# Optimization experiments

Measured on AMD Instinct MI355X. Metric: run time of the kernel, lower is better.

The kernel has to match this reference:

```python
import jax, jax.numpy as jnp
import numpy as np

B = 64
D_MODEL = 2048
D_SSM = 4096      # expand * d_model
HEADDIM = 64
NHEADS = 64       # D_SSM // HEADDIM
D_STATE = 128
D_IN_PROJ = 2 * D_SSM + 2 * D_STATE + NHEADS  # 8512, d_mlp == 0
ACT_LEVELS = 2 ** (8 - 1) - 1  # 127
W_LEVELS = 2 ** (8 - 1) - 1


def fake_quant(x, levels):
    # symmetric absmax fake-quant along last dim with straight-through estimator
    scale = jnp.max(jnp.abs(x), axis=-1, keepdims=True) / levels
    scale = jnp.where(scale == 0, 1.0, scale)
    q = jnp.round(x / scale) * scale
    return x + jax.lax.stop_gradient(q - x)


def quant_linear(x, W):
    # QuantLinear: fake-quant activations (per row) and weights (per output channel)
    xq = fake_quant(x, ACT_LEVELS)
    Wq = fake_quant(W, W_LEVELS)
    return xq @ Wq.T


def softplus_taylor3(x):
    return jnp.log(2.0) + 0.5 * x + x ** 2 / 8.0 + x ** 3 / 48.0


def exp_taylor5(x):
    return 1.0 + x + x ** 2 / 2.0 + x ** 3 / 6.0 + x ** 4 / 24.0 + x ** 5 / 120.0


def setup_inputs() -> dict:
    key = jax.random.key(0)
    k = jax.random.split(key, 7)
    hidden_states = jax.random.normal(k[0], (B, 1, D_MODEL), dtype=jnp.float32)
    ssm_state = jax.random.normal(k[1], (B, NHEADS, HEADDIM, D_STATE), dtype=jnp.float32) * 0.1
    W_in = jax.random.normal(k[2], (D_IN_PROJ, D_MODEL), dtype=jnp.float32) * (1.0 / np.sqrt(D_MODEL))
    # dt_bias = inverse-softplus of dt ~ LogUniform(1e-3, 1e-1)
    dt = jnp.exp(jax.random.uniform(k[3], (NHEADS,)) * (np.log(0.1) - np.log(0.001)) + np.log(0.001))
    dt_bias = dt + jnp.log(-jnp.expm1(-dt))
    A_log = jnp.log(jax.random.uniform(k[4], (NHEADS,), minval=1.0, maxval=16.0))
    Dp = jnp.ones((D_SSM,), dtype=jnp.float32)
    W_out = jax.random.normal(k[5], (D_MODEL, D_SSM), dtype=jnp.float32) * (1.0 / np.sqrt(D_SSM))
    return {"hidden_states": hidden_states, "ssm_state": ssm_state, "W_in": W_in,
            "dt_bias": dt_bias, "A_log": A_log, "D": Dp, "W_out": W_out}


def reference(hidden_states, ssm_state, W_in, dt_bias, A_log, D, W_out):
    dtype = hidden_states.dtype
    b = hidden_states.shape[0]
    zxbcdt = quant_linear(hidden_states[:, 0, :], W_in)  # [b, 8512]
    z = zxbcdt[:, :D_SSM]
    xBC = zxbcdt[:, D_SSM:2 * D_SSM + 2 * D_STATE]
    dt = zxbcdt[:, -NHEADS:]
    # activation fake-quant on xBC (STE)
    xBC = fake_quant(xBC, ACT_LEVELS)
    x = xBC[:, :D_SSM]                                   # [b, d_ssm]
    Bm = xBC[:, D_SSM:D_SSM + D_STATE]                   # [b, n]
    C = xBC[:, D_SSM + D_STATE:]                         # [b, n]
    A = -jnp.exp(A_log.astype(jnp.float32))              # [h]
    # no_sftplus: piecewise 3rd-order Taylor softplus
    dt = dt + dt_bias.astype(dt.dtype)
    dt = jnp.where(dt < -2.0, 0.0, jnp.where(dt > 2.0, dt, softplus_taylor3(dt)))
    # taylor_exp: clipped 5th-order Taylor exp of dt*A
    dA = jnp.maximum(dt * A, -10000.0)
    scale = jnp.clip(exp_taylor5(dA), 0.0, 1.0)          # [b, h]
    xh = x.reshape(b, NHEADS, HEADDIM)                   # [b, h, p]
    dBx = jnp.einsum('bh,bn,bhp->bhpn', dt, Bm, xh)
    ssm_state = ssm_state * scale[:, :, None, None] + dBx  # [b, h, p, n]
    y = jnp.einsum('bhpn,bn->bhp', ssm_state.astype(dtype), C).reshape(b, D_SSM)
    y = fake_quant(y, ACT_LEVELS)
    y = y + D.astype(dtype) * x                          # per-channel skip (D has d_ssm entries)
    y = y * jax.nn.relu(z)
    y = fake_quant(y, ACT_LEVELS)
    out = quant_linear(y, W_out)                         # [b, d_model]
    return out[:, None, :]
```

## Files before the change

kernel.cpp:

```cpp
#include <hip/hip_runtime.h>


#define B_       64
#define DMODEL   2048
#define DSSM     4096
#define NH       64
#define HD       64
#define DSTATE   128
#define DPROJ    8512
#define XBCLEN   4352
#define KS1      1

typedef __attribute__((ext_vector_type(4))) int int4v;

__device__ __forceinline__ float blockMax256(float v, float* sm) {
  #pragma unroll
  for (int off = 32; off > 0; off >>= 1)
    v = fmaxf(v, __shfl_xor(v, off, 64));
  __syncthreads();
  if ((threadIdx.x & 63) == 0) sm[threadIdx.x >> 6] = v;
  __syncthreads();
  return fmaxf(fmaxf(sm[0], sm[1]), fmaxf(sm[2], sm[3]));
}

__device__ __forceinline__ float absmax4(float4 v) {
  return fmaxf(fmaxf(fabsf(v.x), fabsf(v.y)), fmaxf(fabsf(v.z), fabsf(v.w)));
}

__device__ __forceinline__ unsigned int pack4(float a, float b, float c, float d,
                                              float rs) {
  int c0 = (int)rintf(a * rs), c1 = (int)rintf(b * rs);
  int c2 = (int)rintf(c * rs), c3 = (int)rintf(d * rs);
  return (unsigned)(c0 & 255) | ((unsigned)(c1 & 255) << 8) |
         ((unsigned)(c2 & 255) << 16) | ((unsigned)(c3 & 255) << 24);
}

__global__ __launch_bounds__(256) void quantx(const float* __restrict__ in,
                                              unsigned int* __restrict__ outq,
                                              float* __restrict__ scales) {
  __shared__ float sm[4];
  int r = blockIdx.x;
  const float4* row = (const float4*)(in + (size_t)r * DMODEL);
  float4 v[2];
  float m = 0.f;
  #pragma unroll
  for (int i = 0; i < 2; i++) {
    v[i] = row[threadIdx.x + i * 256];
    m = fmaxf(m, absmax4(v[i]));
  }
  float mx = blockMax256(m, sm);
  float s = mx * (1.0f / 127.0f);
  float rs = (s == 0.f) ? 0.f : 127.0f / mx;
  if (s == 0.f) s = 1.f;
  if (threadIdx.x == 0) scales[r] = s;
  unsigned int* orow = outq + (size_t)r * (DMODEL / 4);
  #pragma unroll
  for (int i = 0; i < 2; i++)
    orow[threadIdx.x + i * 256] = pack4(v[i].x, v[i].y, v[i].z, v[i].w, rs);
}

template<int K, int ROWS>
__global__ __launch_bounds__(256) void fgemm(const float* __restrict__ W,
                                             const char* __restrict__ Aq,
                                             const float* __restrict__ sA,
                                             float* __restrict__ Cout, int N) {
  constexpr int NF4 = K / 256;
  constexpr int RPW = ROWS / 4;
  constexpr int LSTRIDE = K / 4 + 4;
  __shared__ unsigned int wq[ROWS * LSTRIDE];
  __shared__ float smax[ROWS];
  int t = threadIdx.x, wave = t >> 6, lane = t & 63;
  int n0 = blockIdx.x * ROWS;
  #pragma unroll
  for (int rr = 0; rr < RPW; rr++) {
    int row = wave * RPW + rr;
    const float4* rp = (const float4*)(W + (size_t)(n0 + row) * K);
    float4 v[NF4];
    float m = 0.f;
    #pragma unroll
    for (int c = 0; c < NF4; c++) {
      v[c] = rp[lane + c * 64];
      m = fmaxf(m, absmax4(v[c]));
    }
    #pragma unroll
    for (int off = 32; off > 0; off >>= 1)
      m = fmaxf(m, __shfl_xor(m, off, 64));
    float s = (m == 0.f) ? 1.f : m * (1.0f / 127.0f);
    float rs = (m == 0.f) ? 0.f : 127.0f / m;
    if (lane == 0) smax[row] = s;
    unsigned int* wrow = wq + row * LSTRIDE;
    #pragma unroll
    for (int c = 0; c < NF4; c++)
      wrow[lane + c * 64] = pack4(v[c].x, v[c].y, v[c].z, v[c].w, rs);
  }
  __syncthreads();
  int l16 = lane & 15, quad = lane >> 4;
  int4v acc = {0, 0, 0, 0};
  const char* arow = Aq + (size_t)(wave * 16 + l16) * K + quad * 16;
  const unsigned int* brow = wq + l16 * LSTRIDE + quad * 4;
  for (int k = 0; k < K; k += 256) {
    int4v af[4], bf[4];
    #pragma unroll
    for (int u = 0; u < 4; u++)
      af[u] = *(const int4v*)(arow + k + u * 64);
    #pragma unroll
    for (int u = 0; u < 4; u++) {
      int4v z = {0, 0, 0, 0};
      bf[u] = z;
      if (l16 < ROWS) bf[u] = *(const int4v*)(brow + (k + u * 64) / 4);
    }
    #pragma unroll
    for (int u = 0; u < 4; u++)
      acc = __builtin_amdgcn_mfma_i32_16x16x64_i8(af[u], bf[u], acc, 0, 0, 0);
  }
  if (l16 < ROWS) {
    float sw = smax[l16];
    #pragma unroll
    for (int r = 0; r < 4; r++) {
      int m = wave * 16 + quad * 4 + r;
      Cout[(size_t)m * N + n0 + l16] = (float)acc[r] * sA[m] * sw;
    }
  }
}

__global__ __launch_bounds__(256) void kmid(
    const float* __restrict__ P1, const float* __restrict__ dt_bias,
    const float* __restrict__ A_log,
    float* __restrict__ zbuf, float* __restrict__ xbcq, float* __restrict__ coefs) {
  __shared__ float sm[4];
  __shared__ float dts[NH];
  __shared__ float sbc;
  int b = blockIdx.x, t = threadIdx.x;
  float4 v[9];
  float m = 0.f;
  #pragma unroll
  for (int i = 0; i < 9; i++) {
    int idx = t + i * 256;
    if (idx < 2128) {
      const float4* p0 = (const float4*)P1 + (size_t)b * 2128 + idx;
      float4 a = p0[0];
      #pragma unroll
      for (int s = 1; s < KS1; s++) {
        float4 q = p0[(size_t)s * 64 * 2128];
        a.x += q.x; a.y += q.y; a.z += q.z; a.w += q.w;
      }
      v[i] = a;
      if (idx >= 1024 && idx < 2112) m = fmaxf(m, absmax4(a));
      if (idx >= 2112) {
        dts[(t - 64) * 4 + 0] = a.x;
        dts[(t - 64) * 4 + 1] = a.y;
        dts[(t - 64) * 4 + 2] = a.z;
        dts[(t - 64) * 4 + 3] = a.w;
      }
    }
  }
  float mx = blockMax256(m, sm);
  float s = mx * (1.0f / 127.0f);
  float rs = (s == 0.f) ? 0.f : 127.0f / mx;
  if (s == 0.f) s = 1.f;
  float4 q8 = {0.f, 0.f, 0.f, 0.f};
  #pragma unroll
  for (int i = 0; i < 9; i++) {
    int idx = t + i * 256;
    if (idx < 1024) {
      *((float4*)(zbuf + (size_t)b * DSSM) + idx) = v[i];
    } else if (idx < 2112) {
      float4 q;
      q.x = rintf(v[i].x * rs) * s;
      q.y = rintf(v[i].y * rs) * s;
      q.z = rintf(v[i].z * rs) * s;
      q.w = rintf(v[i].w * rs) * s;
      if (i == 8) q8 = q;
      *((float4*)(xbcq + (size_t)b * XBCLEN) + (idx - 1024)) = q;
    }
  }
  float4 oth;
  oth.x = __shfl(q8.x, (t & 63) ^ 32, 64);
  oth.y = __shfl(q8.y, (t & 63) ^ 32, 64);
  oth.z = __shfl(q8.z, (t & 63) ^ 32, 64);
  oth.w = __shfl(q8.w, (t & 63) ^ 32, 64);
  float p = 0.f;
  if (t < 32) p = q8.x * oth.x + q8.y * oth.y + q8.z * oth.z + q8.w * oth.w;
  #pragma unroll
  for (int off = 1; off < 32; off <<= 1) p += __shfl_xor(p, off, 64);
  if (t == 0) sbc = p;
  __syncthreads();
  if (t < NH) {
    float dtv = dts[t] + dt_bias[t];
    if (dtv < -2.f) dtv = 0.f;
    else if (dtv <= 2.f)
      dtv = 0.6931471805599453f + 0.5f * dtv + dtv * dtv * (1.f / 8.f)
            + dtv * dtv * dtv * (1.f / 48.f);
    float A = -expf(A_log[t]);
    float dA = fmaxf(dtv * A, -10000.f);
    float e = 1.f + dA + dA * dA * (1.f / 2.f) + dA * dA * dA * (1.f / 6.f)
              + dA * dA * dA * dA * (1.f / 24.f)
              + dA * dA * dA * dA * dA * (1.f / 120.f);
    e = fminf(fmaxf(e, 0.f), 1.f);
    coefs[((size_t)b * NH + t) * 2 + 0] = e;
    coefs[((size_t)b * NH + t) * 2 + 1] = dtv * sbc;
  }
}

__global__ __launch_bounds__(256) void ky(const float* __restrict__ state,
                                          const float* __restrict__ xbcq,
                                          const float* __restrict__ coefs,
                                          float* __restrict__ yraw) {
  int h = blockIdx.x, b = blockIdx.y, t = threadIdx.x;
  const float* xrow = xbcq + (size_t)b * XBCLEN;
  const float* Cv = xrow + DSSM + DSTATE;
  float4 c4 = *(const float4*)(Cv + (t & 31) * 4);
  float2 cf = *(const float2*)(coefs + ((size_t)b * NH + h) * 2);
  const float4* st = (const float4*)(state + ((size_t)b * NH + h) * (HD * DSTATE));
  #pragma unroll
  for (int j = 0; j < 8; j++) {
    float4 s4 = st[j * 256 + t];
    float acc = s4.x * c4.x + s4.y * c4.y + s4.z * c4.z + s4.w * c4.w;
    #pragma unroll
    for (int off = 1; off < 32; off <<= 1) acc += __shfl_xor(acc, off, 64);
    if ((t & 31) == 0) {
      int r = j * 8 + (t >> 5);
      int d = h * HD + r;
      yraw[(size_t)b * DSSM + d] = cf.x * acc + cf.y * xrow[d];
    }
  }
}

__global__ __launch_bounds__(256) void kepi(const float* __restrict__ yraw,
                                            const float* __restrict__ zbuf,
                                            const float* __restrict__ xbcq,
                                            const float* __restrict__ Dv,
                                            unsigned int* __restrict__ q3,
                                            float* __restrict__ sy) {
  __shared__ float sm[4];
  int b = blockIdx.x, t = threadIdx.x;
  const float* yrow = yraw + (size_t)b * DSSM;
  float4 yv[4];
  float m = 0.f;
  #pragma unroll
  for (int i = 0; i < 4; i++) {
    yv[i] = *(const float4*)(yrow + t * 4 + i * 1024);
    m = fmaxf(m, absmax4(yv[i]));
  }
  float mx1 = blockMax256(m, sm);
  float s1 = mx1 * (1.0f / 127.0f);
  float rs1 = (s1 == 0.f) ? 0.f : 127.0f / mx1;
  if (s1 == 0.f) s1 = 1.f;
  float4 y3[4];
  float m2 = 0.f;
  #pragma unroll
  for (int i = 0; i < 4; i++) {
    int idx = t * 4 + i * 1024;
    float4 x4 = *(const float4*)(xbcq + (size_t)b * XBCLEN + idx);
    float4 z4 = *(const float4*)(zbuf + (size_t)b * DSSM + idx);
    float4 d4 = *(const float4*)(Dv + idx);
    float4 r;
    r.x = (rintf(yv[i].x * rs1) * s1 + d4.x * x4.x) * fmaxf(z4.x, 0.f);
    r.y = (rintf(yv[i].y * rs1) * s1 + d4.y * x4.y) * fmaxf(z4.y, 0.f);
    r.z = (rintf(yv[i].z * rs1) * s1 + d4.z * x4.z) * fmaxf(z4.z, 0.f);
    r.w = (rintf(yv[i].w * rs1) * s1 + d4.w * x4.w) * fmaxf(z4.w, 0.f);
    y3[i] = r;
    m2 = fmaxf(m2, absmax4(r));
  }
  float mx3 = blockMax256(m2, sm);
  float s3 = mx3 * (1.0f / 127.0f);
  float rs3 = (s3 == 0.f) ? 0.f : 127.0f / mx3;
  if (s3 == 0.f) s3 = 1.f;
  if (t == 0) sy[b] = s3;
  unsigned int* orow = q3 + (size_t)b * (DSSM / 4);
  #pragma unroll
  for (int i = 0; i < 4; i++)
    orow[t + i * 256] = pack4(y3[i].x, y3[i].y, y3[i].z, y3[i].w, rs3);
}

extern "C" void kernel_launch(void* const* d_in, const int* in_sizes, int n_in,
                              void* d_out, int out_size, void* d_ws, size_t ws_size,
                              hipStream_t stream) {
  const float* hidden  = (const float*)d_in[0];
  const float* ssm     = (const float*)d_in[1];
  const float* W_in    = (const float*)d_in[2];
  const float* dt_bias = (const float*)d_in[3];
  const float* A_log   = (const float*)d_in[4];
  const float* Dv      = (const float*)d_in[5];
  const float* W_out   = (const float*)d_in[6];
  float* out = (float*)d_out;

  char* p = (char*)d_ws;
  auto alloc = [&](size_t bytes) {
    char* r = p;
    p += (bytes + 255) & ~(size_t)255;
    return r;
  };
  unsigned int* xq = (unsigned int*)alloc((size_t)B_ * DMODEL);
  unsigned int* q3 = (unsigned int*)alloc((size_t)B_ * DSSM);
  float* sx    = (float*)alloc(B_ * 4);
  float* sy    = (float*)alloc(B_ * 4);
  float* zxb   = (float*)alloc((size_t)B_ * DPROJ * 4);
  float* zbuf  = (float*)alloc((size_t)B_ * DSSM * 4);
  float* xbcq  = (float*)alloc((size_t)B_ * XBCLEN * 4);
  float* coefs = (float*)alloc((size_t)B_ * NH * 2 * 4);
  float* yraw  = (float*)alloc((size_t)B_ * DSSM * 4);

  quantx<<<B_, 256, 0, stream>>>(hidden, xq, sx);
  fgemm<DMODEL, 16><<<DPROJ / 16, 256, 0, stream>>>(W_in, (const char*)xq, sx,
                                                    zxb, DPROJ);
  kmid<<<B_, 256, 0, stream>>>(zxb, dt_bias, A_log, zbuf, xbcq, coefs);
  ky<<<dim3(NH, B_), 256, 0, stream>>>(ssm, xbcq, coefs, yraw);
  kepi<<<B_, 256, 0, stream>>>(yraw, zbuf, xbcq, Dv, q3, sy);
  fgemm<DSSM, 4><<<DMODEL / 4, 256, 0, stream>>>(W_out, (const char*)q3, sy,
                                                 out, DMODEL);
}
```

Before: 306.7 us.

## Split W_out row quantization across 512 threads, shrink W_in tile, batch ky loads

Adds a 512-thread output-projection GEMM where two waves share each weight row's absmax and int8 packing, halving per-wave load depth before the MFMA stage. The input-projection GEMM now uses 8-row tiles instead of 16, doubling the block count so more CUs take part. The ky kernel issues all eight state loads up front and interleaves the shuffle reductions to raise memory-level parallelism. The unused split-K summation in kmid is also removed. The costs are an extra block barrier, more register pressure in ky, and more blocks for the first GEMM.

```diff
diff --git a/kernel.cpp b/kernel.cpp
--- a/kernel.cpp
+++ b/kernel.cpp
@@ -9,7 +9,7 @@
 #define DSTATE   128
 #define DPROJ    8512
 #define XBCLEN   4352
-#define KS1      1
+#define LSTRIDE2 (DSSM / 4 + 4)
 
 typedef __attribute__((ext_vector_type(4))) int int4v;
 
@@ -25,6 +25,13 @@
 
 __device__ __forceinline__ float absmax4(float4 v) {
   return fmaxf(fmaxf(fabsf(v.x), fabsf(v.y)), fmaxf(fabsf(v.z), fabsf(v.w)));
+}
+
+__device__ __forceinline__ float waveMax(float v) {
+  #pragma unroll
+  for (int off = 32; off > 0; off >>= 1)
+    v = fmaxf(v, __shfl_xor(v, off, 64));
+  return v;
 }
 
 __device__ __forceinline__ unsigned int pack4(float a, float b, float c, float d,
@@ -82,9 +89,7 @@
       v[c] = rp[lane + c * 64];
       m = fmaxf(m, absmax4(v[c]));
     }
-    #pragma unroll
-    for (int off = 32; off > 0; off >>= 1)
-      m = fmaxf(m, __shfl_xor(m, off, 64));
+    m = waveMax(m);
     float s = (m == 0.f) ? 1.f : m * (1.0f / 127.0f);
     float rs = (m == 0.f) ? 0.f : 127.0f / m;
     if (lane == 0) smax[row] = s;
@@ -119,6 +124,70 @@
     for (int r = 0; r < 4; r++) {
       int m = wave * 16 + quad * 4 + r;
       Cout[(size_t)m * N + n0 + l16] = (float)acc[r] * sA[m] * sw;
+    }
+  }
+}
+
+__global__ __launch_bounds__(512) void fgemm2k(const float* __restrict__ W,
+                                               const char* __restrict__ Aq,
+                                               const float* __restrict__ sA,
+                                               float* __restrict__ Cout) {
+  __shared__ unsigned int wq[4 * LSTRIDE2];
+  __shared__ float smax[4];
+  __shared__ float hmax[4][2];
+  int t = threadIdx.x, wave = t >> 6, lane = t & 63;
+  int l16 = lane & 15, quad = lane >> 4;
+  int n0 = blockIdx.x * 4;
+  {
+    int row = wave >> 1, kh = wave & 1;
+    const float4* rp = (const float4*)(W + (size_t)(n0 + row) * DSSM);
+    float4 v[8];
+    float m = 0.f;
+    #pragma unroll
+    for (int c = 0; c < 8; c++) {
+      v[c] = rp[lane + (kh * 8 + c) * 64];
+      m = fmaxf(m, absmax4(v[c]));
+    }
+    m = waveMax(m);
+    if (lane == 0) hmax[row][kh] = m;
+    __syncthreads();
+    float mm = fmaxf(hmax[row][0], hmax[row][1]);
+    float s = (mm == 0.f) ? 1.f : mm * (1.0f / 127.0f);
+    float rs = (mm == 0.f) ? 0.f : 127.0f / mm;
+    if (lane == 0 && kh == 0) smax[row] = s;
+    unsigned int* wrow = wq + row * LSTRIDE2;
+    #pragma unroll
+    for (int c = 0; c < 8; c++)
+      wrow[lane + (kh * 8 + c) * 64] = pack4(v[c].x, v[c].y, v[c].z, v[c].w, rs);
+  }
+  __syncthreads();
+  if (wave < 4) {
+    int m4 = wave;
+    int4v acc = {0, 0, 0, 0};
+    const char* arow = Aq + (size_t)(m4 * 16 + l16) * DSSM + quad * 16;
+    const unsigned int* brow = wq + l16 * LSTRIDE2 + quad * 4;
+    for (int k = 0; k < DSSM; k += 256) {
+      int4v af[4], bf[4];
+      #pragma unroll
+      for (int u = 0; u < 4; u++)
+        af[u] = *(const int4v*)(arow + k + u * 64);
+      #pragma unroll
+      for (int u = 0; u < 4; u++) {
+        int4v z = {0, 0, 0, 0};
+        bf[u] = z;
+        if (l16 < 4) bf[u] = *(const int4v*)(brow + (k + u * 64) / 4);
+      }
+      #pragma unroll
+      for (int u = 0; u < 4; u++)
+        acc = __builtin_amdgcn_mfma_i32_16x16x64_i8(af[u], bf[u], acc, 0, 0, 0);
+    }
+    if (l16 < 4) {
+      float sw = smax[l16];
+      #pragma unroll
+      for (int r = 0; r < 4; r++) {
+        int mr = m4 * 16 + quad * 4 + r;
+        Cout[(size_t)mr * DMODEL + n0 + l16] = (float)acc[r] * sA[mr] * sw;
+      }
     }
   }
 }
@@ -137,13 +206,7 @@
   for (int i = 0; i < 9; i++) {
     int idx = t + i * 256;
     if (idx < 2128) {
-      const float4* p0 = (const float4*)P1 + (size_t)b * 2128 + idx;
-      float4 a = p0[0];
-      #pragma unroll
-      for (int s = 1; s < KS1; s++) {
-        float4 q = p0[(size_t)s * 64 * 2128];
-        a.x += q.x; a.y += q.y; a.z += q.z; a.w += q.w;
-      }
+      float4 a = ((const float4*)P1)[(size_t)b * 2128 + idx];
       v[i] = a;
       if (idx >= 1024 && idx < 2112) m = fmaxf(m, absmax4(a));
       if (idx >= 2112) {
@@ -212,16 +275,24 @@
   float4 c4 = *(const float4*)(Cv + (t & 31) * 4);
   float2 cf = *(const float2*)(coefs + ((size_t)b * NH + h) * 2);
   const float4* st = (const float4*)(state + ((size_t)b * NH + h) * (HD * DSTATE));
-  #pragma unroll
-  for (int j = 0; j < 8; j++) {
-    float4 s4 = st[j * 256 + t];
-    float acc = s4.x * c4.x + s4.y * c4.y + s4.z * c4.z + s4.w * c4.w;
-    #pragma unroll
-    for (int off = 1; off < 32; off <<= 1) acc += __shfl_xor(acc, off, 64);
-    if ((t & 31) == 0) {
+  float4 s4[8];
+  #pragma unroll
+  for (int j = 0; j < 8; j++) s4[j] = st[j * 256 + t];
+  float acc[8];
+  #pragma unroll
+  for (int j = 0; j < 8; j++)
+    acc[j] = s4[j].x * c4.x + s4[j].y * c4.y + s4[j].z * c4.z + s4[j].w * c4.w;
+  #pragma unroll
+  for (int off = 1; off < 32; off <<= 1) {
+    #pragma unroll
+    for (int j = 0; j < 8; j++) acc[j] += __shfl_xor(acc[j], off, 64);
+  }
+  if ((t & 31) == 0) {
+    #pragma unroll
+    for (int j = 0; j < 8; j++) {
       int r = j * 8 + (t >> 5);
       int d = h * HD + r;
-      yraw[(size_t)b * DSSM + d] = cf.x * acc + cf.y * xrow[d];
+      yraw[(size_t)b * DSSM + d] = cf.x * acc[j] + cf.y * xrow[d];
     }
   }
 }
@@ -302,11 +373,10 @@
   float* yraw  = (float*)alloc((size_t)B_ * DSSM * 4);
 
   quantx<<<B_, 256, 0, stream>>>(hidden, xq, sx);
-  fgemm<DMODEL, 16><<<DPROJ / 16, 256, 0, stream>>>(W_in, (const char*)xq, sx,
-                                                    zxb, DPROJ);
+  fgemm<DMODEL, 8><<<DPROJ / 8, 256, 0, stream>>>(W_in, (const char*)xq, sx,
+                                                  zxb, DPROJ);
   kmid<<<B_, 256, 0, stream>>>(zxb, dt_bias, A_log, zbuf, xbcq, coefs);
   ky<<<dim3(NH, B_), 256, 0, stream>>>(ssm, xbcq, coefs, yraw);
   kepi<<<B_, 256, 0, stream>>>(yraw, zbuf, xbcq, Dv, q3, sy);
-  fgemm<DSSM, 4><<<DMODEL / 4, 256, 0, stream>>>(W_out, (const char*)q3, sy,
-                                                 out, DMODEL);
-}
+  fgemm2k<<<DMODEL / 4, 512, 0, stream>>>(W_out, (const char*)q3, sy, out);
+}
```

New measurement: 311.3 us. Within noise of the previous version (+1.5%).
